# Performance work log

Hardware: AMD Instinct MI355X
Metric: run time of the kernel (lower is better)

Reference implementation:

```python
import jax, jax.numpy as jnp
import numpy as np

N_NODES = 100000
N_EDGES = 1600000
HIDDEN = 128
MAX_DEG = 64
EPS = 1e-6


def setup_inputs() -> dict:
    key = jax.random.key(0)
    ks = jax.random.split(key, 6)
    x = jax.random.randint(ks[0], (N_NODES,), 0, MAX_DEG + 1)
    edge_index = jax.random.randint(ks[1], (2, N_EDGES), 0, N_NODES)
    edge_weight = jax.random.uniform(ks[2], (N_EDGES,), dtype=jnp.float32)
    emb = jax.random.normal(ks[3], (MAX_DEG + 1, HIDDEN), dtype=jnp.float32)
    # 5 GraphNorms in application order: emb_gn, conv0.gn, gns[0], conv1.gn, gns[1]
    gn_weight = jax.random.uniform(ks[4], (5, HIDDEN), dtype=jnp.float32)
    gn_bias = jnp.zeros((5, HIDDEN), dtype=jnp.float32)
    gn_mean_scale = jax.random.uniform(ks[5], (5, HIDDEN), dtype=jnp.float32)
    return {"x": x, "edge_index": edge_index, "edge_weight": edge_weight,
            "emb": emb, "gn_weight": gn_weight, "gn_bias": gn_bias,
            "gn_mean_scale": gn_mean_scale}


def _graphnorm(h, w, b, ms):
    # GLASS GraphNorm over the whole node set (single-graph batch)
    mean = jnp.mean(h, axis=0)              # [D]
    out = h - mean * ms                     # [N,D]
    std = jnp.sqrt(jnp.mean(out * out, axis=0) + EPS)
    return w * out / std + b


def reference(x, edge_index, edge_weight, emb, gn_weight, gn_bias, gn_mean_scale):
    row, col = edge_index[0], edge_index[1]
    n = N_NODES
    # mean-aggregated normalized adjacency (buildAdj, aggr='mean')
    deg = jax.ops.segment_sum(edge_weight, row, num_segments=n)
    deg = jnp.where(deg < 0.5, deg + 1.0, deg)
    w_norm = edge_weight / deg[row]         # [E]

    def spmm(h):
        # (adj @ h)[i] = sum_{e: row[e]=i} w_norm[e] * h[col[e]]
        return jax.ops.segment_sum(h[col] * w_norm[:, None], row, num_segments=n)

    # input embedding + emb_gn (dropout is identity in eval mode)
    h = emb[x]                              # [N, HIDDEN]
    h = _graphnorm(h, gn_weight[0], gn_bias[0], gn_mean_scale[0])
    # layer 0: GLASSConv (adj @ h -> gn) then outer gns[0] and ReLU
    h = spmm(h)
    h = _graphnorm(h, gn_weight[1], gn_bias[1], gn_mean_scale[1])
    h = _graphnorm(h, gn_weight[2], gn_bias[2], gn_mean_scale[2])
    h = jax.nn.relu(h)
    # layer 1 (last conv) then final gns[-1]; jk=False -> take last
    h = spmm(h)
    h = _graphnorm(h, gn_weight[3], gn_bias[3], gn_mean_scale[3])
    h = _graphnorm(h, gn_weight[4], gn_bias[4], gn_mean_scale[4])
    return h
```

## Files before the change

kernel.cpp:

```cpp
#include <hip/hip_runtime.h>

#define HID 128
#define EPSF 1e-6f

__device__ inline unsigned f2bf(float f) {
  unsigned u = __float_as_uint(f);
  return (u + 0x7fffu + ((u >> 16) & 1u)) >> 16;
}

__global__ void k_hist(const int* __restrict__ x, int n, int* __restrict__ hist) {
  __shared__ int lh[65];
  int t = threadIdx.x;
  if (t < 65) lh[t] = 0;
  __syncthreads();
  for (int i = blockIdx.x * blockDim.x + t; i < n; i += gridDim.x * blockDim.x)
    atomicAdd(&lh[x[i]], 1);
  __syncthreads();
  if (t < 65 && lh[t]) atomicAdd(&hist[t], lh[t]);
}

__global__ void k_cnt(const int* __restrict__ row, int e, int* __restrict__ cnt) {
  for (int i = blockIdx.x * blockDim.x + threadIdx.x; i < e; i += gridDim.x * blockDim.x)
    atomicAdd(&cnt[row[i]], 1);
}

__global__ void k_scan_partial(const int* __restrict__ cnt, int n, int* __restrict__ bsum) {
  __shared__ int sh[256];
  int t = threadIdx.x;
  int base = blockIdx.x * 2048 + t * 8;
  int s = 0;
#pragma unroll
  for (int j = 0; j < 8; ++j) { int idx = base + j; if (idx < n) s += cnt[idx]; }
  sh[t] = s; __syncthreads();
  for (int off = 128; off > 0; off >>= 1) {
    if (t < off) sh[t] += sh[t + off];
    __syncthreads();
  }
  if (t == 0) bsum[blockIdx.x] = sh[0];
}

__global__ void k_scan_bsum(int* __restrict__ bsum, int nb) {
  if (threadIdx.x == 0 && blockIdx.x == 0) {
    int acc = 0;
    for (int i = 0; i < nb; ++i) { int v = bsum[i]; bsum[i] = acc; acc += v; }
  }
}

__global__ void k_scan_final(const int* __restrict__ cnt, int n, const int* __restrict__ bsum,
                             int* __restrict__ rowptr, int* __restrict__ cursor) {
  __shared__ int sh[256];
  int t = threadIdx.x;
  int base = blockIdx.x * 2048 + t * 8;
  int v[8]; int s = 0;
#pragma unroll
  for (int j = 0; j < 8; ++j) { int idx = base + j; v[j] = (idx < n) ? cnt[idx] : 0; s += v[j]; }
  sh[t] = s; __syncthreads();
  for (int off = 1; off < 256; off <<= 1) {
    int val = (t >= off) ? sh[t - off] : 0;
    __syncthreads();
    sh[t] += val;
    __syncthreads();
  }
  int off0 = bsum[blockIdx.x] + sh[t] - s;
#pragma unroll
  for (int j = 0; j < 8; ++j) {
    int idx = base + j;
    if (idx < n) { rowptr[idx] = off0; cursor[idx] = off0; off0 += v[j]; }
  }
}

__global__ void k_scatter(const int* __restrict__ row, const int* __restrict__ col,
                          const float* __restrict__ ew, const int* __restrict__ x, int e,
                          int* __restrict__ cursor, int2* __restrict__ sedge) {
  for (int i = blockIdx.x * blockDim.x + threadIdx.x; i < e; i += gridDim.x * blockDim.x) {
    int r = row[i];
    int c = col[i];
    int xc = x[c];
    int pos = atomicAdd(&cursor[r], 1);
    sedge[pos] = make_int2(c | (xc << 17), __float_as_int(ew[i]));
  }
}

__global__ void k_gn0(const float* __restrict__ emb, const int* __restrict__ hist,
                      const float* __restrict__ gw, const float* __restrict__ gb,
                      const float* __restrict__ gms, float invN,
                      float* __restrict__ emb1) {
  int d = threadIdx.x;
  float s = 0.f, s2 = 0.f;
  for (int k = 0; k < 65; ++k) {
    float v = emb[k * HID + d];
    float c = (float)hist[k];
    s += c * v; s2 += c * v * v;
  }
  float m = s * invN, E2 = s2 * invN;
  float ms0 = gms[d], w0 = gw[d], b0 = gb[d];
  float sh = m * ms0;
  float a = w0 / sqrtf(E2 - 2.f * sh * m + sh * sh + EPSF);
  float c = b0 - a * sh;
  for (int k = 0; k < 65; ++k) emb1[k * HID + d] = fmaf(a, emb[k * HID + d], c);
}

__global__ void k_gnchain(const float* __restrict__ gsum, const float* __restrict__ gsq,
                          float invN, const float* __restrict__ gw, const float* __restrict__ gb,
                          const float* __restrict__ gms, int i1, int i2,
                          float* __restrict__ A, float* __restrict__ C) {
  int d = threadIdx.x;
  float m = gsum[d] * invN, E2 = gsq[d] * invN;
  float ms1 = gms[i1 * HID + d], w1 = gw[i1 * HID + d], b1 = gb[i1 * HID + d];
  float sh1 = m * ms1;
  float a1 = w1 / sqrtf(E2 - 2.f * sh1 * m + sh1 * sh1 + EPSF);
  float c1 = b1 - a1 * sh1;
  float m2 = a1 * m + c1;
  float E2b = a1 * a1 * E2 + 2.f * a1 * c1 * m + c1 * c1;
  float ms2 = gms[i2 * HID + d], w2 = gw[i2 * HID + d], b2 = gb[i2 * HID + d];
  float sh2 = m2 * ms2;
  float a2 = w2 / sqrtf(E2b - 2.f * sh2 * m2 + sh2 * sh2 + EPSF);
  float c2 = b2 - a2 * sh2;
  A[d] = a2 * a1;
  C[d] = a2 * c1 + c2;
}

__global__ __launch_bounds__(256) void k_spmm1(
    const int* __restrict__ rowptr, const int2* __restrict__ sedge,
    const float* __restrict__ emb1, int n, int nwaves,
    unsigned* __restrict__ h2b, float* __restrict__ gsum, float* __restrict__ gsq) {
  __shared__ float lemb[65 * HID];
  __shared__ float red[2][4][64][2];
  int t = threadIdx.x;
  for (int i = t; i < 65 * HID; i += 256) lemb[i] = emb1[i];
  __syncthreads();
  int l = t & 63, wv = t >> 6;
  int gwid = blockIdx.x * 4 + wv;
  float ps0 = 0, ps1 = 0, q0 = 0, q1 = 0;
  for (int node = gwid; node < n; node += nwaves) {
    int nd = __builtin_amdgcn_readfirstlane(node);
    int p0 = rowptr[nd], p1 = rowptr[nd + 1];
    float wsum = 0.f, a0 = 0.f, a1 = 0.f;
    int p = p0;
    int nfull = p0 + ((p1 - p0) & ~7);
    for (; p < nfull; p += 8) {
      int2 b[8];
#pragma unroll
      for (int k = 0; k < 8; ++k) b[k] = sedge[p + k];
#pragma unroll
      for (int k = 0; k < 8; ++k) {
        int xc = b[k].x >> 17;
        float w = __int_as_float(b[k].y);
        const float2 v = *(const float2*)&lemb[xc * HID + l * 2];
        wsum += w;
        a0 = fmaf(w, v.x, a0);
        a1 = fmaf(w, v.y, a1);
      }
    }
    for (; p < p1; ++p) {
      int2 b = sedge[p];
      int xc = b.x >> 17;
      float w = __int_as_float(b.y);
      const float2 v = *(const float2*)&lemb[xc * HID + l * 2];
      wsum += w;
      a0 = fmaf(w, v.x, a0);
      a1 = fmaf(w, v.y, a1);
    }
    float d = (wsum < 0.5f) ? wsum + 1.0f : wsum;
    float invd = 1.0f / d;
    a0 *= invd; a1 *= invd;
    h2b[(size_t)node * (HID / 2) + l] = f2bf(a0) | (f2bf(a1) << 16);
    ps0 += a0; ps1 += a1; q0 += a0 * a0; q1 += a1 * a1;
  }
  red[0][wv][l][0] = ps0; red[0][wv][l][1] = ps1;
  red[1][wv][l][0] = q0;  red[1][wv][l][1] = q1;
  __syncthreads();
  if (wv == 0) {
    float s0 = 0, s1 = 0, t0 = 0, t1 = 0;
#pragma unroll
    for (int k = 0; k < 4; ++k) {
      s0 += red[0][k][l][0]; s1 += red[0][k][l][1];
      t0 += red[1][k][l][0]; t1 += red[1][k][l][1];
    }
    atomicAdd(&gsum[l * 2], s0); atomicAdd(&gsum[l * 2 + 1], s1);
    atomicAdd(&gsq[l * 2], t0);  atomicAdd(&gsq[l * 2 + 1], t1);
  }
}

__global__ __launch_bounds__(256) void k_spmm2(
    const int* __restrict__ rowptr, const int2* __restrict__ sedge,
    const unsigned* __restrict__ h2b,
    const float* __restrict__ A, const float* __restrict__ C,
    int n, int nwaves, float* __restrict__ out,
    float* __restrict__ gsum, float* __restrict__ gsq) {
  __shared__ float red[2][4][64][2];
  int t = threadIdx.x;
  int l = t & 63, wv = t >> 6;
  int gwid = blockIdx.x * 4 + wv;
  float A0 = A[l * 2], A1 = A[l * 2 + 1], C0 = C[l * 2], C1 = C[l * 2 + 1];
  float ps0 = 0, ps1 = 0, q0 = 0, q1 = 0;
  for (int node = gwid; node < n; node += nwaves) {
    int nd = __builtin_amdgcn_readfirstlane(node);
    int p0 = rowptr[nd], p1 = rowptr[nd + 1];
    float wsum = 0.f, a0 = 0.f, a1 = 0.f;
    int cntf = (p1 - p0) >> 3;
    int p = p0;
    int2 b[8], nb[8];
    if (cntf) {
#pragma unroll
      for (int k = 0; k < 8; ++k) b[k] = sedge[p + k];
    }
    for (int it = 0; it < cntf; ++it) {
      unsigned u[8];
#pragma unroll
      for (int k = 0; k < 8; ++k) {
        int c = b[k].x & 0x1FFFF;
        u[k] = h2b[(size_t)c * (HID / 2) + l];
      }
      p += 8;
      if (it + 1 < cntf) {
#pragma unroll
        for (int k = 0; k < 8; ++k) nb[k] = sedge[p + k];
      }
#pragma unroll
      for (int k = 0; k < 8; ++k) {
        float w = __int_as_float(b[k].y);
        wsum += w;
        float h0 = __uint_as_float(u[k] << 16);
        float h1 = __uint_as_float(u[k] & 0xFFFF0000u);
        a0 = fmaf(w, fmaxf(fmaf(A0, h0, C0), 0.f), a0);
        a1 = fmaf(w, fmaxf(fmaf(A1, h1, C1), 0.f), a1);
      }
#pragma unroll
      for (int k = 0; k < 8; ++k) b[k] = nb[k];
    }
    for (; p < p1; ++p) {
      int2 e = sedge[p];
      int c = e.x & 0x1FFFF;
      unsigned uu = h2b[(size_t)c * (HID / 2) + l];
      float w = __int_as_float(e.y);
      wsum += w;
      float h0 = __uint_as_float(uu << 16);
      float h1 = __uint_as_float(uu & 0xFFFF0000u);
      a0 = fmaf(w, fmaxf(fmaf(A0, h0, C0), 0.f), a0);
      a1 = fmaf(w, fmaxf(fmaf(A1, h1, C1), 0.f), a1);
    }
    float d = (wsum < 0.5f) ? wsum + 1.0f : wsum;
    float invd = 1.0f / d;
    a0 *= invd; a1 *= invd;
    *(float2*)&out[(size_t)node * HID + l * 2] = make_float2(a0, a1);
    ps0 += a0; ps1 += a1; q0 += a0 * a0; q1 += a1 * a1;
  }
  red[0][wv][l][0] = ps0; red[0][wv][l][1] = ps1;
  red[1][wv][l][0] = q0;  red[1][wv][l][1] = q1;
  __syncthreads();
  if (wv == 0) {
    float s0 = 0, s1 = 0, t0 = 0, t1 = 0;
#pragma unroll
    for (int k = 0; k < 4; ++k) {
      s0 += red[0][k][l][0]; s1 += red[0][k][l][1];
      t0 += red[1][k][l][0]; t1 += red[1][k][l][1];
    }
    atomicAdd(&gsum[l * 2], s0); atomicAdd(&gsum[l * 2 + 1], s1);
    atomicAdd(&gsq[l * 2], t0);  atomicAdd(&gsq[l * 2 + 1], t1);
  }
}

__global__ void k_final(float* __restrict__ out, const float* __restrict__ A,
                        const float* __restrict__ C, int n) {
  __shared__ float la[HID], lc[HID];
  if (threadIdx.x < HID) { la[threadIdx.x] = A[threadIdx.x]; lc[threadIdx.x] = C[threadIdx.x]; }
  __syncthreads();
  int total = n * 32;
  for (int i = blockIdx.x * blockDim.x + threadIdx.x; i < total; i += gridDim.x * blockDim.x) {
    float4 v = *(float4*)(out + (size_t)i * 4);
    int cg = (i & 31) * 4;
    v.x = fmaf(la[cg + 0], v.x, lc[cg + 0]);
    v.y = fmaf(la[cg + 1], v.y, lc[cg + 1]);
    v.z = fmaf(la[cg + 2], v.z, lc[cg + 2]);
    v.w = fmaf(la[cg + 3], v.w, lc[cg + 3]);
    *(float4*)(out + (size_t)i * 4) = v;
  }
}

extern "C" void kernel_launch(void* const* d_in, const int* in_sizes, int n_in,
                              void* d_out, int out_size, void* d_ws, size_t ws_size,
                              hipStream_t stream) {
  const int* x = (const int*)d_in[0];
  const int* ei = (const int*)d_in[1];
  const float* ew = (const float*)d_in[2];
  const float* emb = (const float*)d_in[3];
  const float* gw = (const float*)d_in[4];
  const float* gb = (const float*)d_in[5];
  const float* gms = (const float*)d_in[6];
  float* out = (float*)d_out;

  const int n = in_sizes[0];
  const int e = in_sizes[1] / 2;
  const int* row = ei;
  const int* col = ei + e;

  float* wsf = (float*)d_ws;
  size_t o = 0;
  auto alloc = [&](size_t elems) -> size_t { size_t r = o; o += ((elems + 31) & ~(size_t)31); return r; };
  size_t cnt_o = alloc(n + 1);
  size_t hist_o = alloc(65);
  size_t sum2_o = alloc(HID), sq2_o = alloc(HID), sum4_o = alloc(HID), sq4_o = alloc(HID);
  size_t zero_end = o;
  size_t A12_o = alloc(HID), C12_o = alloc(HID), A34_o = alloc(HID), C34_o = alloc(HID);
  size_t rowptr_o = alloc(n + 1);
  size_t cursor_o = alloc(n + 1);
  size_t bsum_o = alloc(64);
  size_t emb1_o = alloc(65 * HID);
  size_t sedge_o = alloc((size_t)e * 2);
  size_t h2b_o = alloc((size_t)n * HID / 2);

  int* cnt = (int*)(wsf + cnt_o);
  int* hist = (int*)(wsf + hist_o);
  float* sum2 = wsf + sum2_o; float* sq2 = wsf + sq2_o;
  float* sum4 = wsf + sum4_o; float* sq4 = wsf + sq4_o;
  float* A12 = wsf + A12_o; float* C12 = wsf + C12_o;
  float* A34 = wsf + A34_o; float* C34 = wsf + C34_o;
  int* rowptr = (int*)(wsf + rowptr_o);
  int* cursor = (int*)(wsf + cursor_o);
  int* bsum = (int*)(wsf + bsum_o);
  float* emb1 = wsf + emb1_o;
  int2* sedge = (int2*)(wsf + sedge_o);
  unsigned* h2b = (unsigned*)(wsf + h2b_o);

  const float invN = 1.0f / (float)n;
  const int nblk = 2048;
  const int nwaves = nblk * 4;

  hipMemsetAsync(d_ws, 0, zero_end * sizeof(float), stream);
  k_hist<<<256, 256, 0, stream>>>(x, n, hist);
  k_cnt<<<2048, 256, 0, stream>>>(row, e, cnt);
  int nb = (n + 1 + 2047) / 2048;
  k_scan_partial<<<nb, 256, 0, stream>>>(cnt, n + 1, bsum);
  k_scan_bsum<<<1, 64, 0, stream>>>(bsum, nb);
  k_scan_final<<<nb, 256, 0, stream>>>(cnt, n + 1, bsum, rowptr, cursor);
  k_scatter<<<2048, 256, 0, stream>>>(row, col, ew, x, e, cursor, sedge);
  k_gn0<<<1, HID, 0, stream>>>(emb, hist, gw, gb, gms, invN, emb1);
  k_spmm1<<<nblk, 256, 0, stream>>>(rowptr, sedge, emb1, n, nwaves, h2b, sum2, sq2);
  k_gnchain<<<1, HID, 0, stream>>>(sum2, sq2, invN, gw, gb, gms, 1, 2, A12, C12);
  k_spmm2<<<nblk, 256, 0, stream>>>(rowptr, sedge, h2b, A12, C12, n, nwaves, out, sum4, sq4);
  k_gnchain<<<1, HID, 0, stream>>>(sum4, sq4, invN, gw, gb, gms, 3, 4, A34, C34);
  k_final<<<2048, 256, 0, stream>>>(out, A34, C34, n);
}
```

Baseline: 567.9 us.

## Quantize layer-1 features to int8 for second SpMM gather, merge hist/count kernels

Adds a per-channel absmax pass in spmm1 and a new quantization kernel that packs the bf16 intermediate features into int8. This halves the bytes spmm2 gathers per edge; the GraphNorm scale is folded into the dequant multiplier. It also stores the normalized embedding table as bf16 in shared memory, fuses the histogram and degree-count kernels, and unrolls the edge scatter by four. The trade is an extra quantization pass and lower precision (int8 with per-channel scale), which adds numerical error to the second layer.

```diff
diff --git a/kernel.cpp b/kernel.cpp
--- a/kernel.cpp
+++ b/kernel.cpp
@@ -7,21 +7,20 @@
   unsigned u = __float_as_uint(f);
   return (u + 0x7fffu + ((u >> 16) & 1u)) >> 16;
 }
-
-__global__ void k_hist(const int* __restrict__ x, int n, int* __restrict__ hist) {
+__device__ inline float bf2f_lo(unsigned u) { return __uint_as_float(u << 16); }
+__device__ inline float bf2f_hi(unsigned u) { return __uint_as_float(u & 0xFFFF0000u); }
+
+__global__ void k_histcnt(const int* __restrict__ x, int n, const int* __restrict__ row,
+                          int e, int* __restrict__ hist, int* __restrict__ cnt) {
   __shared__ int lh[65];
   int t = threadIdx.x;
   if (t < 65) lh[t] = 0;
   __syncthreads();
-  for (int i = blockIdx.x * blockDim.x + t; i < n; i += gridDim.x * blockDim.x)
-    atomicAdd(&lh[x[i]], 1);
+  int tid = blockIdx.x * blockDim.x + t, stride = gridDim.x * blockDim.x;
+  for (int i = tid; i < e; i += stride) atomicAdd(&cnt[row[i]], 1);
+  for (int i = tid; i < n; i += stride) atomicAdd(&lh[x[i]], 1);
   __syncthreads();
   if (t < 65 && lh[t]) atomicAdd(&hist[t], lh[t]);
-}
-
-__global__ void k_cnt(const int* __restrict__ row, int e, int* __restrict__ cnt) {
-  for (int i = blockIdx.x * blockDim.x + threadIdx.x; i < e; i += gridDim.x * blockDim.x)
-    atomicAdd(&cnt[row[i]], 1);
 }
 
 __global__ void k_scan_partial(const int* __restrict__ cnt, int n, int* __restrict__ bsum) {
@@ -69,41 +68,61 @@
   }
 }
 
-__global__ void k_scatter(const int* __restrict__ row, const int* __restrict__ col,
-                          const float* __restrict__ ew, const int* __restrict__ x, int e,
-                          int* __restrict__ cursor, int2* __restrict__ sedge) {
-  for (int i = blockIdx.x * blockDim.x + threadIdx.x; i < e; i += gridDim.x * blockDim.x) {
-    int r = row[i];
-    int c = col[i];
-    int xc = x[c];
-    int pos = atomicAdd(&cursor[r], 1);
-    sedge[pos] = make_int2(c | (xc << 17), __float_as_int(ew[i]));
+__global__ __launch_bounds__(256) void k_scatter(
+    const int* __restrict__ row, const int* __restrict__ col,
+    const float* __restrict__ ew, const int* __restrict__ x, int e,
+    int* __restrict__ cursor, int2* __restrict__ sedge) {
+  int tid = blockIdx.x * blockDim.x + threadIdx.x;
+  int stride = gridDim.x * blockDim.x;
+  for (int i0 = tid; i0 < e; i0 += stride * 4) {
+    int r[4], c[4], xc[4], idx[4]; float w[4]; bool valid[4];
+#pragma unroll
+    for (int k = 0; k < 4; ++k) {
+      int i = i0 + k * stride; valid[k] = (i < e);
+      if (valid[k]) { r[k] = row[i]; c[k] = col[i]; w[k] = ew[i]; }
+    }
+#pragma unroll
+    for (int k = 0; k < 4; ++k) if (valid[k]) xc[k] = x[c[k]];
+#pragma unroll
+    for (int k = 0; k < 4; ++k) if (valid[k]) idx[k] = atomicAdd(&cursor[r[k]], 1);
+#pragma unroll
+    for (int k = 0; k < 4; ++k)
+      if (valid[k]) sedge[idx[k]] = make_int2(c[k] | (xc[k] << 17), __float_as_int(w[k]));
   }
 }
 
 __global__ void k_gn0(const float* __restrict__ emb, const int* __restrict__ hist,
                       const float* __restrict__ gw, const float* __restrict__ gb,
                       const float* __restrict__ gms, float invN,
-                      float* __restrict__ emb1) {
-  int d = threadIdx.x;
-  float s = 0.f, s2 = 0.f;
+                      unsigned* __restrict__ emb1b) {
+  int t = threadIdx.x;
+  int d0 = t * 2, d1 = t * 2 + 1;
+  float s0 = 0, s20 = 0, s1 = 0, s21 = 0;
   for (int k = 0; k < 65; ++k) {
-    float v = emb[k * HID + d];
     float c = (float)hist[k];
-    s += c * v; s2 += c * v * v;
-  }
-  float m = s * invN, E2 = s2 * invN;
-  float ms0 = gms[d], w0 = gw[d], b0 = gb[d];
-  float sh = m * ms0;
-  float a = w0 / sqrtf(E2 - 2.f * sh * m + sh * sh + EPSF);
-  float c = b0 - a * sh;
-  for (int k = 0; k < 65; ++k) emb1[k * HID + d] = fmaf(a, emb[k * HID + d], c);
+    float v0 = emb[k * HID + d0], v1 = emb[k * HID + d1];
+    s0 += c * v0; s20 += c * v0 * v0;
+    s1 += c * v1; s21 += c * v1 * v1;
+  }
+  float m0 = s0 * invN, E20 = s20 * invN;
+  float m1 = s1 * invN, E21 = s21 * invN;
+  float sh0 = m0 * gms[d0], sh1 = m1 * gms[d1];
+  float aa0 = gw[d0] / sqrtf(E20 - 2.f * sh0 * m0 + sh0 * sh0 + EPSF);
+  float aa1 = gw[d1] / sqrtf(E21 - 2.f * sh1 * m1 + sh1 * sh1 + EPSF);
+  float cc0 = gb[d0] - aa0 * sh0, cc1 = gb[d1] - aa1 * sh1;
+  for (int k = 0; k < 65; ++k) {
+    float y0 = fmaf(aa0, emb[k * HID + d0], cc0);
+    float y1 = fmaf(aa1, emb[k * HID + d1], cc1);
+    emb1b[k * (HID / 2) + t] = f2bf(y0) | (f2bf(y1) << 16);
+  }
 }
 
 __global__ void k_gnchain(const float* __restrict__ gsum, const float* __restrict__ gsq,
                           float invN, const float* __restrict__ gw, const float* __restrict__ gb,
                           const float* __restrict__ gms, int i1, int i2,
-                          float* __restrict__ A, float* __restrict__ C) {
+                          float* __restrict__ A, float* __restrict__ C,
+                          const float* __restrict__ hmax, float* __restrict__ Aq,
+                          float* __restrict__ qinv) {
   int d = threadIdx.x;
   float m = gsum[d] * invN, E2 = gsq[d] * invN;
   float ms1 = gms[i1 * HID + d], w1 = gw[i1 * HID + d], b1 = gb[i1 * HID + d];
@@ -116,22 +135,29 @@
   float sh2 = m2 * ms2;
   float a2 = w2 / sqrtf(E2b - 2.f * sh2 * m2 + sh2 * sh2 + EPSF);
   float c2 = b2 - a2 * sh2;
-  A[d] = a2 * a1;
-  C[d] = a2 * c1 + c2;
+  float Af = a2 * a1, Cf = a2 * c1 + c2;
+  A[d] = Af; C[d] = Cf;
+  if (hmax) {
+    float h = hmax[d];
+    Aq[d] = Af * (h * (1.0f / 127.0f));
+    qinv[d] = (h > 0.f) ? 127.0f / h : 0.f;
+  }
 }
 
 __global__ __launch_bounds__(256) void k_spmm1(
     const int* __restrict__ rowptr, const int2* __restrict__ sedge,
-    const float* __restrict__ emb1, int n, int nwaves,
-    unsigned* __restrict__ h2b, float* __restrict__ gsum, float* __restrict__ gsq) {
-  __shared__ float lemb[65 * HID];
+    const unsigned* __restrict__ emb1b, int n, int nwaves,
+    unsigned* __restrict__ h2b, float* __restrict__ gsum, float* __restrict__ gsq,
+    unsigned* __restrict__ hmax) {
+  __shared__ unsigned lemb[65 * 64];
   __shared__ float red[2][4][64][2];
-  int t = threadIdx.x;
-  for (int i = t; i < 65 * HID; i += 256) lemb[i] = emb1[i];
+  __shared__ float rmx[4][64][2];
+  int t = threadIdx.x;
+  for (int i = t; i < 65 * 64; i += 256) lemb[i] = emb1b[i];
   __syncthreads();
   int l = t & 63, wv = t >> 6;
   int gwid = blockIdx.x * 4 + wv;
-  float ps0 = 0, ps1 = 0, q0 = 0, q1 = 0;
+  float ps0 = 0, ps1 = 0, q0s = 0, q1s = 0, m0 = 0, m1 = 0;
   for (int node = gwid; node < n; node += nwaves) {
     int nd = __builtin_amdgcn_readfirstlane(node);
     int p0 = rowptr[nd], p1 = rowptr[nd + 1];
@@ -144,110 +170,122 @@
       for (int k = 0; k < 8; ++k) b[k] = sedge[p + k];
 #pragma unroll
       for (int k = 0; k < 8; ++k) {
-        int xc = b[k].x >> 17;
+        unsigned v = lemb[(unsigned)(b[k].x >> 17) * 64 + l];
         float w = __int_as_float(b[k].y);
-        const float2 v = *(const float2*)&lemb[xc * HID + l * 2];
         wsum += w;
-        a0 = fmaf(w, v.x, a0);
-        a1 = fmaf(w, v.y, a1);
+        a0 = fmaf(w, bf2f_lo(v), a0);
+        a1 = fmaf(w, bf2f_hi(v), a1);
       }
     }
     for (; p < p1; ++p) {
       int2 b = sedge[p];
-      int xc = b.x >> 17;
+      unsigned v = lemb[(unsigned)(b.x >> 17) * 64 + l];
       float w = __int_as_float(b.y);
-      const float2 v = *(const float2*)&lemb[xc * HID + l * 2];
       wsum += w;
-      a0 = fmaf(w, v.x, a0);
-      a1 = fmaf(w, v.y, a1);
+      a0 = fmaf(w, bf2f_lo(v), a0);
+      a1 = fmaf(w, bf2f_hi(v), a1);
     }
     float d = (wsum < 0.5f) ? wsum + 1.0f : wsum;
     float invd = 1.0f / d;
     a0 *= invd; a1 *= invd;
-    h2b[(size_t)node * (HID / 2) + l] = f2bf(a0) | (f2bf(a1) << 16);
-    ps0 += a0; ps1 += a1; q0 += a0 * a0; q1 += a1 * a1;
+    unsigned b0 = f2bf(a0), b1 = f2bf(a1);
+    h2b[(size_t)node * 64 + l] = b0 | (b1 << 16);
+    m0 = fmaxf(m0, fabsf(__uint_as_float(b0 << 16)));
+    m1 = fmaxf(m1, fabsf(__uint_as_float(b1 << 16)));
+    ps0 += a0; ps1 += a1; q0s += a0 * a0; q1s += a1 * a1;
   }
   red[0][wv][l][0] = ps0; red[0][wv][l][1] = ps1;
-  red[1][wv][l][0] = q0;  red[1][wv][l][1] = q1;
+  red[1][wv][l][0] = q0s; red[1][wv][l][1] = q1s;
+  rmx[wv][l][0] = m0; rmx[wv][l][1] = m1;
   __syncthreads();
   if (wv == 0) {
-    float s0 = 0, s1 = 0, t0 = 0, t1 = 0;
+    float s0 = 0, s1 = 0, t0 = 0, t1 = 0, x0 = 0, x1 = 0;
 #pragma unroll
     for (int k = 0; k < 4; ++k) {
       s0 += red[0][k][l][0]; s1 += red[0][k][l][1];
       t0 += red[1][k][l][0]; t1 += red[1][k][l][1];
+      x0 = fmaxf(x0, rmx[k][l][0]); x1 = fmaxf(x1, rmx[k][l][1]);
     }
     atomicAdd(&gsum[l * 2], s0); atomicAdd(&gsum[l * 2 + 1], s1);
     atomicAdd(&gsq[l * 2], t0);  atomicAdd(&gsq[l * 2 + 1], t1);
+    atomicMax(&hmax[l * 2], __float_as_uint(x0));
+    atomicMax(&hmax[l * 2 + 1], __float_as_uint(x1));
+  }
+}
+
+__global__ __launch_bounds__(256) void k_quant(const unsigned* __restrict__ h2b,
+                                               const float* __restrict__ qinv, int n,
+                                               unsigned* __restrict__ qmat) {
+  int stride = gridDim.x * blockDim.x;
+  int total = n * 32;
+  for (int idx = blockIdx.x * blockDim.x + threadIdx.x; idx < total; idx += stride) {
+    int node = idx >> 5, g = idx & 31;
+    const unsigned* src = &h2b[(size_t)node * 64 + g * 2];
+    unsigned v0 = src[0], v1 = src[1];
+    float4 qv = *(const float4*)&qinv[g * 4];
+    int c0 = (int)rintf(bf2f_lo(v0) * qv.x);
+    int c1 = (int)rintf(bf2f_hi(v0) * qv.y);
+    int c2 = (int)rintf(bf2f_lo(v1) * qv.z);
+    int c3 = (int)rintf(bf2f_hi(v1) * qv.w);
+    qmat[idx] = (unsigned)(c0 & 0xFF) | ((unsigned)(c1 & 0xFF) << 8) |
+                ((unsigned)(c2 & 0xFF) << 16) | ((unsigned)(c3 & 0xFF) << 24);
   }
 }
 
 __global__ __launch_bounds__(256) void k_spmm2(
     const int* __restrict__ rowptr, const int2* __restrict__ sedge,
-    const unsigned* __restrict__ h2b,
-    const float* __restrict__ A, const float* __restrict__ C,
+    const unsigned char* __restrict__ qmat,
+    const float* __restrict__ Aq, const float* __restrict__ C,
     int n, int nwaves, float* __restrict__ out,
     float* __restrict__ gsum, float* __restrict__ gsq) {
   __shared__ float red[2][4][64][2];
   int t = threadIdx.x;
   int l = t & 63, wv = t >> 6;
   int gwid = blockIdx.x * 4 + wv;
-  float A0 = A[l * 2], A1 = A[l * 2 + 1], C0 = C[l * 2], C1 = C[l * 2 + 1];
-  float ps0 = 0, ps1 = 0, q0 = 0, q1 = 0;
+  float A0 = Aq[l * 2], A1 = Aq[l * 2 + 1], C0 = C[l * 2], C1 = C[l * 2 + 1];
+  float ps0 = 0, ps1 = 0, q0s = 0, q1s = 0;
   for (int node = gwid; node < n; node += nwaves) {
     int nd = __builtin_amdgcn_readfirstlane(node);
     int p0 = rowptr[nd], p1 = rowptr[nd + 1];
     float wsum = 0.f, a0 = 0.f, a1 = 0.f;
-    int cntf = (p1 - p0) >> 3;
     int p = p0;
-    int2 b[8], nb[8];
-    if (cntf) {
+    int nfull = p0 + ((p1 - p0) & ~7);
+    for (; p < nfull; p += 8) {
+      int2 b[8];
 #pragma unroll
       for (int k = 0; k < 8; ++k) b[k] = sedge[p + k];
-    }
-    for (int it = 0; it < cntf; ++it) {
-      unsigned u[8];
-#pragma unroll
-      for (int k = 0; k < 8; ++k) {
-        int c = b[k].x & 0x1FFFF;
-        u[k] = h2b[(size_t)c * (HID / 2) + l];
-      }
-      p += 8;
-      if (it + 1 < cntf) {
-#pragma unroll
-        for (int k = 0; k < 8; ++k) nb[k] = sedge[p + k];
-      }
+      unsigned short u[8];
+#pragma unroll
+      for (int k = 0; k < 8; ++k)
+        u[k] = *(const unsigned short*)&qmat[(size_t)(b[k].x & 0x1FFFF) * 128 + l * 2];
 #pragma unroll
       for (int k = 0; k < 8; ++k) {
         float w = __int_as_float(b[k].y);
         wsum += w;
-        float h0 = __uint_as_float(u[k] << 16);
-        float h1 = __uint_as_float(u[k] & 0xFFFF0000u);
-        a0 = fmaf(w, fmaxf(fmaf(A0, h0, C0), 0.f), a0);
-        a1 = fmaf(w, fmaxf(fmaf(A1, h1, C1), 0.f), a1);
+        float y0 = fmaxf(fmaf(A0, (float)(signed char)(u[k] & 0xFF), C0), 0.f);
+        float y1 = fmaxf(fmaf(A1, (float)(signed char)(u[k] >> 8), C1), 0.f);
+        a0 = fmaf(w, y0, a0);
+        a1 = fmaf(w, y1, a1);
       }
-#pragma unroll
-      for (int k = 0; k < 8; ++k) b[k] = nb[k];
     }
     for (; p < p1; ++p) {
-      int2 e = sedge[p];
-      int c = e.x & 0x1FFFF;
-      unsigned uu = h2b[(size_t)c * (HID / 2) + l];
-      float w = __int_as_float(e.y);
+      int2 b = sedge[p];
+      unsigned short u = *(const unsigned short*)&qmat[(size_t)(b.x & 0x1FFFF) * 128 + l * 2];
+      float w = __int_as_float(b.y);
       wsum += w;
-      float h0 = __uint_as_float(uu << 16);
-      float h1 = __uint_as_float(uu & 0xFFFF0000u);
-      a0 = fmaf(w, fmaxf(fmaf(A0, h0, C0), 0.f), a0);
-      a1 = fmaf(w, fmaxf(fmaf(A1, h1, C1), 0.f), a1);
+      float y0 = fmaxf(fmaf(A0, (float)(signed char)(u & 0xFF), C0), 0.f);
+      float y1 = fmaxf(fmaf(A1, (float)(signed char)(u >> 8), C1), 0.f);
+      a0 = fmaf(w, y0, a0);
+      a1 = fmaf(w, y1, a1);
     }
     float d = (wsum < 0.5f) ? wsum + 1.0f : wsum;
     float invd = 1.0f / d;
     a0 *= invd; a1 *= invd;
     *(float2*)&out[(size_t)node * HID + l * 2] = make_float2(a0, a1);
-    ps0 += a0; ps1 += a1; q0 += a0 * a0; q1 += a1 * a1;
+    ps0 += a0; ps1 += a1; q0s += a0 * a0; q1s += a1 * a1;
   }
   red[0][wv][l][0] = ps0; red[0][wv][l][1] = ps1;
-  red[1][wv][l][0] = q0;  red[1][wv][l][1] = q1;
+  red[1][wv][l][0] = q0s; red[1][wv][l][1] = q1s;
   __syncthreads();
   if (wv == 0) {
     float s0 = 0, s1 = 0, t0 = 0, t1 = 0;
@@ -301,44 +339,53 @@
   size_t cnt_o = alloc(n + 1);
   size_t hist_o = alloc(65);
   size_t sum2_o = alloc(HID), sq2_o = alloc(HID), sum4_o = alloc(HID), sq4_o = alloc(HID);
+  size_t hmax_o = alloc(HID);
   size_t zero_end = o;
   size_t A12_o = alloc(HID), C12_o = alloc(HID), A34_o = alloc(HID), C34_o = alloc(HID);
+  size_t Aq_o = alloc(HID), qinv_o = alloc(HID);
   size_t rowptr_o = alloc(n + 1);
   size_t cursor_o = alloc(n + 1);
   size_t bsum_o = alloc(64);
-  size_t emb1_o = alloc(65 * HID);
+  size_t emb1b_o = alloc(65 * HID / 2);
   size_t sedge_o = alloc((size_t)e * 2);
   size_t h2b_o = alloc((size_t)n * HID / 2);
+  size_t qmat_o = alloc((size_t)n * HID / 4);
 
   int* cnt = (int*)(wsf + cnt_o);
   int* hist = (int*)(wsf + hist_o);
   float* sum2 = wsf + sum2_o; float* sq2 = wsf + sq2_o;
   float* sum4 = wsf + sum4_o; float* sq4 = wsf + sq4_o;
+  unsigned* hmax = (unsigned*)(wsf + hmax_o);
   float* A12 = wsf + A12_o; float* C12 = wsf + C12_o;
   float* A34 = wsf + A34_o; float* C34 = wsf + C34_o;
+  float* Aq = wsf + Aq_o; float* qinv = wsf + qinv_o;
   int* rowptr = (int*)(wsf + rowptr_o);
   int* cursor = (int*)(wsf + cursor_o);
   int* bsum = (int*)(wsf + bsum_o);
-  float* emb1 = wsf + emb1_o;
+  unsigned* emb1b = (unsigned*)(wsf + emb1b_o);
   int2* sedge = (int2*)(wsf + sedge_o);
   unsigned* h2b = (unsigned*)(wsf + h2b_o);
+  unsigned* qmat = (unsigned*)(wsf + qmat_o);
 
   const float invN = 1.0f / (float)n;
   const int nblk = 2048;
   const int nwaves = nblk * 4;
 
   hipMemsetAsync(d_ws, 0, zero_end * sizeof(float), stream);
-  k_hist<<<256, 256, 0, stream>>>(x, n, hist);
-  k_cnt<<<2048, 256, 0, stream>>>(row, e, cnt);
+  k_histcnt<<<2048, 256, 0, stream>>>(x, n, row, e, hist, cnt);
   int nb = (n + 1 + 2047) / 2048;
   k_scan_partial<<<nb, 256, 0, stream>>>(cnt, n + 1, bsum);
   k_scan_bsum<<<1, 64, 0, stream>>>(bsum, nb);
   k_scan_final<<<nb, 256, 0, stream>>>(cnt, n + 1, bsum, rowptr, cursor);
   k_scatter<<<2048, 256, 0, stream>>>(row, col, ew, x, e, cursor, sedge);
-  k_gn0<<<1, HID, 0, stream>>>(emb, hist, gw, gb, gms, invN, emb1);
-  k_spmm1<<<nblk, 256, 0, stream>>>(rowptr, sedge, emb1, n, nwaves, h2b, sum2, sq2);
-  k_gnchain<<<1, HID, 0, stream>>>(sum2, sq2, invN, gw, gb, gms, 1, 2, A12, C12);
-  k_spmm2<<<nblk, 256, 0, stream>>>(rowptr, sedge, h2b, A12, C12, n, nwaves, out, sum4, sq4);
-  k_gnchain<<<1, HID, 0, stream>>>(sum4, sq4, invN, gw, gb, gms, 3, 4, A34, C34);
+  k_gn0<<<1, 64, 0, stream>>>(emb, hist, gw, gb, gms, invN, emb1b);
+  k_spmm1<<<nblk, 256, 0, stream>>>(rowptr, sedge, emb1b, n, nwaves, h2b, sum2, sq2, hmax);
+  k_gnchain<<<1, HID, 0, stream>>>(sum2, sq2, invN, gw, gb, gms, 1, 2, A12, C12,
+                                   (const float*)hmax, Aq, qinv);
+  k_quant<<<2048, 256, 0, stream>>>(h2b, qinv, n, qmat);
+  k_spmm2<<<nblk, 256, 0, stream>>>(rowptr, sedge, (const unsigned char*)qmat, Aq, C12,
+                                    n, nwaves, out, sum4, sq4);
+  k_gnchain<<<1, HID, 0, stream>>>(sum4, sq4, invN, gw, gb, gms, 3, 4, A34, C34,
+                                   nullptr, nullptr, nullptr);
   k_final<<<2048, 256, 0, stream>>>(out, A34, C34, n);
 }
```

Result: slower. 587.3 us (+3.4%).
